# Optimization experiments

Measured on AMD Instinct MI355X. Metric: run time of the kernel, lower is better.

Reference implementation:

```python
import jax, jax.numpy as jnp
import numpy as np

N_HEAD = 16
ROPE_BASE = 10000.0


def _rope_tables(T, head_dim, dtype=jnp.float32):
    inv_freq = 1.0 / (ROPE_BASE ** (jnp.arange(0, head_dim, 2, dtype=jnp.float32) / head_dim))
    t = jnp.arange(T, dtype=jnp.float32)
    freqs = t[:, None] * inv_freq[None, :]          # [T, D/2]
    emb = jnp.concatenate([freqs, freqs], axis=-1)  # [T, D]
    return jnp.cos(emb).astype(dtype), jnp.sin(emb).astype(dtype)


def _rotate_half(x):
    d = x.shape[-1] // 2
    return jnp.concatenate([-x[..., d:], x[..., :d]], axis=-1)


def setup_inputs() -> dict:
    key = jax.random.key(0)
    ks = jax.random.split(key, 5)
    B, T, C = 2, 2048, 2048
    s = 1.0 / np.sqrt(C)
    return {
        "x": jax.random.normal(ks[0], (B, T, C), dtype=jnp.float32),
        "wq": jax.random.normal(ks[1], (C, C), dtype=jnp.float32) * s,
        "wk": jax.random.normal(ks[2], (C, C), dtype=jnp.float32) * s,
        "wv": jax.random.normal(ks[3], (C, C), dtype=jnp.float32) * s,
        "wo": jax.random.normal(ks[4], (C, C), dtype=jnp.float32) * s,
    }


def reference(x, wq, wk, wv, wo):
    B, T, C = x.shape
    H = N_HEAD
    D = C // H

    def heads(y):  # [B,T,C] -> [B,H,T,D]
        return y.reshape(B, T, H, D).transpose(0, 2, 1, 3)

    q = heads(x @ wq)
    k = heads(x @ wk)
    v = heads(x @ wv)

    cos, sin = _rope_tables(T, D, x.dtype)          # [T, D]
    cos = cos[None, None, :, :]
    sin = sin[None, None, :, :]
    q = q * cos + _rotate_half(q) * sin
    k = k * cos + _rotate_half(k) * sin

    scale = 1.0 / np.sqrt(D)
    scores = jnp.einsum('bhqd,bhkd->bhqk', q, k) * scale   # [B,H,T,T]
    causal = jnp.tril(jnp.ones((T, T), dtype=bool))
    scores = jnp.where(causal[None, None, :, :], scores, jnp.finfo(scores.dtype).min)
    attn = jax.nn.softmax(scores, axis=-1)
    y = jnp.einsum('bhqk,bhkd->bhqd', attn, v)             # [B,H,T,D]
    y = y.transpose(0, 2, 1, 3).reshape(B, T, C)
    return y @ wo
```

## Files before the change

### kernel.cpp

```cpp
#include <hip/hip_runtime.h>
#include <hip/hip_bf16.h>
#include <math.h>


#define TT 2048
#define CCn 2048
#define HH 16
#define DD 128
#define MMr 4096
#define NQKV 6144

typedef __attribute__((ext_vector_type(8))) short s16x8;
typedef __attribute__((ext_vector_type(4))) short s16x4;
typedef __attribute__((ext_vector_type(4))) float f32x4;

__device__ __forceinline__ short bf16_of(float f) {
  unsigned u = __float_as_uint(f);
  unsigned r = u + 0x7fffu + ((u >> 16) & 1u);
  return (short)(r >> 16);
}
__device__ __forceinline__ float f_of_bf16(short s) {
  return __uint_as_float(((unsigned)(unsigned short)s) << 16);
}
__device__ __forceinline__ float ex2(float x) { return exp2f(x); }

__device__ __forceinline__ void lds_load16(const void* g, void* l) {
  __builtin_amdgcn_global_load_lds((__attribute__((address_space(1))) void*)g,
                                   (__attribute__((address_space(3))) void*)l,
                                   16, 0, 0);
}

__global__ __launch_bounds__(256) void k_tables(float* __restrict__ cosT,
                                                float* __restrict__ sinT) {
  int idx = blockIdx.x * 256 + threadIdx.x;
  int t = idx >> 6, i = idx & 63;
  float inv = powf(10000.0f, -(float)i * (1.0f / 64.0f));
  float f = (float)t * inv;
  cosT[idx] = cosf(f);
  sinT[idx] = sinf(f);
}

__global__ __launch_bounds__(256) void k_cast_x(const float* __restrict__ x,
                                                short* __restrict__ xb) {
  int i = blockIdx.x * 256 + threadIdx.x;
  f32x4 v = ((const f32x4*)x)[i];
  s16x4 o;
#pragma unroll
  for (int j = 0; j < 4; ++j) o[j] = bf16_of(v[j]);
  ((s16x4*)xb)[i] = o;
}

__global__ __launch_bounds__(256) void k_wtrans4(const float* __restrict__ w0,
                                                 const float* __restrict__ w1,
                                                 const float* __restrict__ w2,
                                                 const float* __restrict__ w3,
                                                 short* __restrict__ wqkvT,
                                                 short* __restrict__ woT) {
  __shared__ float tile[32][33];
  int z = blockIdx.z;
  const float* w = (z == 0) ? w0 : (z == 1) ? w1 : (z == 2) ? w2 : w3;
  short* wt = (z == 3) ? woT : wqkvT + (size_t)z * 2048 * 2048;
  int n0 = blockIdx.x * 32, k0 = blockIdx.y * 32;
  int tx = threadIdx.x & 31, ty = threadIdx.x >> 5;
#pragma unroll
  for (int j = 0; j < 4; ++j) {
    int k = ty * 4 + j;
    tile[k][tx] = w[(size_t)(k0 + k) * CCn + n0 + tx];
  }
  __syncthreads();
#pragma unroll
  for (int j = 0; j < 4; ++j) {
    int n = ty * 4 + j;
    wt[(size_t)(n0 + n) * CCn + k0 + tx] = bf16_of(tile[tx][n]);
  }
}

__global__ __launch_bounds__(256) void k_vtrans(const short* __restrict__ src,
                                                short* __restrict__ dst) {
  __shared__ short tile[32][33];
  int bh = blockIdx.y, b = bh >> 4, h = bh & 15;
  int dt = blockIdx.x & 3, tt = blockIdx.x >> 2;
  int tx = threadIdx.x & 31, ty = threadIdx.x >> 5;
  const short* sp = src + ((size_t)(b * TT + tt * 32)) * NQKV + 4096 + h * DD + dt * 32;
#pragma unroll
  for (int j = 0; j < 4; ++j) {
    int tr = ty * 4 + j;
    tile[tr][tx] = sp[(size_t)tr * NQKV + tx];
  }
  __syncthreads();
  short* dp = dst + ((size_t)(bh * DD + dt * 32)) * TT + tt * 32;
#pragma unroll
  for (int j = 0; j < 4; ++j) {
    int dr = ty * 4 + j;
    dp[(size_t)dr * TT + tx] = tile[tx][dr];
  }
}

__global__ __launch_bounds__(256) void k_rope2(const short* __restrict__ qkv,
                                               const float* __restrict__ cosT,
                                               const float* __restrict__ sinT,
                                               short* __restrict__ Qb,
                                               short* __restrict__ Kb, float kmul) {
  int which = blockIdx.y;
  int coff = which << 11;
  short* dstb = which ? Kb : Qb;
  float mul = which ? kmul : 1.0f;
  int idx = blockIdx.x * 256 + threadIdx.x;
  int i4 = (idx & 15) * 4;
  int h = (idx >> 4) & 15;
  int t = (idx >> 8) & 2047;
  int b = idx >> 19;
  const short* row = qkv + ((size_t)(b * TT + t)) * NQKV + coff + h * DD;
  s16x4 v0 = *(const s16x4*)(row + i4);
  s16x4 v1 = *(const s16x4*)(row + i4 + 64);
  f32x4 c4 = *(const f32x4*)(cosT + t * 64 + i4);
  f32x4 s4 = *(const f32x4*)(sinT + t * 64 + i4);
  s16x4 o0, o1;
#pragma unroll
  for (int j = 0; j < 4; ++j) {
    float a = f_of_bf16(v0[j]), bb = f_of_bf16(v1[j]);
    o0[j] = bf16_of((a * c4[j] - bb * s4[j]) * mul);
    o1[j] = bf16_of((bb * c4[j] + a * s4[j]) * mul);
  }
  short* orow = dstb + ((size_t)((b * HH + h) * TT + t)) * DD;
  *(s16x4*)(orow + i4) = o0;
  *(s16x4*)(orow + i4 + 64) = o1;
}

template <int BF, int BSTG, bool BF16OUT>
__global__ __launch_bounds__(512) void k_gemmW(const short* __restrict__ A,
                                               const short* __restrict__ Bt,
                                               void* __restrict__ Cout,
                                               int M, int N, int K) {
  constexpr int BN = BF * 64;
  constexpr int AH = 4096;
  constexpr int BH = BN * 32;
  __shared__ short smem[4 * AH + 4 * BH];
  const int tid = threadIdx.x, wid = tid >> 6, lane = tid & 63;
  const int wm = wid >> 2, wn = wid & 3;
  const int lr = lane & 15, lk = lane >> 4;
  const int swz = (lk ^ ((lr >> 1) & 3)) * 8;

  int nwg = gridDim.x, orig = blockIdx.x;
  int xcd = orig & 7, bidx = orig >> 3;
  int q = nwg >> 3, rmd = nwg & 7;
  int wg = (xcd < rmd) ? (xcd * (q + 1) + bidx)
                       : (rmd * (q + 1) + (xcd - rmd) * q + bidx);
  const int NBM = M >> 7;
  const int m0 = (wg % NBM) * 128, n0 = (wg / NBM) * BN;

  const int ldswave = (tid & ~63) * 8;

  auto stageA = [&](int buf, int h, int kt) {
    int rr = tid >> 2, cs = tid & 3;
    int cc = cs ^ ((rr >> 1) & 3);
    lds_load16(A + (size_t)(m0 + rr) * K + kt * 64 + h * 32 + cc * 8,
               smem + buf * 2 * AH + h * AH + ldswave);
  };
  auto stageB = [&](int buf, int h, int kt) {
#pragma unroll
    for (int l = 0; l < BSTG; ++l) {
      int lin = l * 512 + tid;
      int rr = lin >> 2, cs = lin & 3;
      int cc = cs ^ ((rr >> 1) & 3);
      lds_load16(Bt + (size_t)(n0 + rr) * K + kt * 64 + h * 32 + cc * 8,
                 smem + 4 * AH + buf * 2 * BH + h * BH + l * 4096 + ldswave);
    }
  };

  s16x8 af[4], bfr[BF / 2];
  f32x4 acc[4][BF] = {};

#define LOAD_A(ks, buf)                                                        \
  _Pragma("unroll") for (int i = 0; i < 4; ++i) af[i] =                        \
      *(const s16x8*)(smem + (buf) * 2 * AH + (ks) * AH +                      \
                      (wm * 64 + i * 16 + lr) * 32 + swz);
#define LOAD_B(ks, bh, buf)                                                    \
  _Pragma("unroll") for (int j = 0; j < BF / 2; ++j) bfr[j] =                  \
      *(const s16x8*)(smem + 4 * AH + (buf) * 2 * BH + (ks) * BH +             \
                      (wn * (BF * 16) + ((bh) * (BF / 2) + j) * 16 + lr) * 32 +\
                      swz);
#define PHASE_MFMA(bh)                                                         \
  __builtin_amdgcn_s_setprio(1);                                               \
  _Pragma("unroll") for (int i = 0; i < 4; ++i)                                \
      _Pragma("unroll") for (int j = 0; j < BF / 2; ++j)                       \
      acc[i][(bh) * (BF / 2) + j] = __builtin_amdgcn_mfma_f32_16x16x32_bf16(   \
          af[i], bfr[j], acc[i][(bh) * (BF / 2) + j], 0, 0, 0);                \
  __builtin_amdgcn_s_setprio(0);
#define VMCNT_N()                                                              \
  if constexpr (BSTG == 3) asm volatile("s_waitcnt vmcnt(4)" ::: "memory");    \
  else asm volatile("s_waitcnt vmcnt(3)" ::: "memory");

  const int nk = K >> 6;
  stageA(0, 0, 0);
  stageB(0, 0, 0);
  stageA(0, 1, 0);
  stageB(0, 1, 0);
  stageA(1, 0, 1);
  stageB(1, 0, 1);
  VMCNT_N();
  __builtin_amdgcn_s_barrier();

#pragma unroll 1
  for (int kt = 0; kt < nk; ++kt) {
    const int buf = kt & 1, nbuf = buf ^ 1;
    const bool s1 = (kt + 1 < nk), s2 = (kt + 2 < nk);
    LOAD_A(0, buf);
    LOAD_B(0, 0, buf);
    if (s1) stageA(nbuf, 1, kt + 1);
    __builtin_amdgcn_s_barrier();
    PHASE_MFMA(0);
    __builtin_amdgcn_s_barrier();
    LOAD_B(0, 1, buf);
    if (s1) stageB(nbuf, 1, kt + 1);
    __builtin_amdgcn_s_barrier();
    PHASE_MFMA(1);
    __builtin_amdgcn_s_barrier();
    LOAD_A(1, buf);
    LOAD_B(1, 0, buf);
    if (s2) stageA(buf, 0, kt + 2);
    __builtin_amdgcn_s_barrier();
    PHASE_MFMA(0);
    __builtin_amdgcn_s_barrier();
    LOAD_B(1, 1, buf);
    if (s2) stageB(buf, 0, kt + 2);
    __builtin_amdgcn_s_barrier();
    PHASE_MFMA(1);
    if (kt < nk - 2) {
      VMCNT_N();
    } else {
      asm volatile("s_waitcnt vmcnt(0)" ::: "memory");
    }
    __builtin_amdgcn_s_barrier();
  }
#undef LOAD_A
#undef LOAD_B
#undef PHASE_MFMA
#undef VMCNT_N

#pragma unroll
  for (int i = 0; i < 4; ++i)
#pragma unroll
    for (int j = 0; j < BF; ++j) {
      int row0 = m0 + wm * 64 + i * 16 + lk * 4;
      int col = n0 + wn * (BF * 16) + j * 16 + lr;
#pragma unroll
      for (int rr = 0; rr < 4; ++rr) {
        if (BF16OUT)
          ((short*)Cout)[(size_t)(row0 + rr) * N + col] = bf16_of(acc[i][j][rr]);
        else
          ((float*)Cout)[(size_t)(row0 + rr) * N + col] = acc[i][j][rr];
      }
    }
}

__global__ __launch_bounds__(256) void k_attn(const short* __restrict__ Qb,
                                              const short* __restrict__ Kb,
                                              const short* __restrict__ Vt,
                                              short* __restrict__ yb) {
  __shared__ short Ks[2][64 * 128];
  __shared__ short Vs[128 * 64];
  __shared__ short Ps[4][16 * 72];
  const int tid = threadIdx.x, wid = tid >> 6, lane = tid & 63;
  const int lr = lane & 15, lk = lane >> 4;
  const int bh = blockIdx.y, bx = blockIdx.x;
  const size_t baseQK = (size_t)bh * TT * DD;
  const int b = bh >> 4, h = bh & 15;

  auto stageK = [&](int bi, int kt2) {
#pragma unroll
    for (int it = 0; it < 4; ++it) {
      int ch = it * 256 + tid;
      int r = ch >> 4, cc = ch & 15;
      int cs = cc ^ (r & 7);
      lds_load16(Kb + baseQK + (size_t)(kt2 * 64 + r) * DD + cs * 8,
                 &Ks[bi][(size_t)(it * 256 + wid * 64) * 8]);
    }
  };
  auto stageV = [&](int kt2) {
#pragma unroll
    for (int it = 0; it < 4; ++it) {
      int ch = it * 256 + tid;
      int d = ch >> 3, kc = ch & 7;
      int cs = kc ^ (d & 7);
      lds_load16(Vt + baseQK + (size_t)d * TT + kt2 * 64 + cs * 8,
                 &Vs[(size_t)(it * 256 + wid * 64) * 8]);
    }
  };

#pragma unroll 1
  for (int pass = 0; pass < 2; ++pass) {
    const int qt = pass ? (31 - bx) : bx;
    const int q0 = qt * 64;
    const int qg = q0 + wid * 16 + lr;
    s16x8 qf[4];
#pragma unroll
    for (int ds = 0; ds < 4; ++ds)
      qf[ds] = *(const s16x8*)(Qb + baseQK + (size_t)qg * DD + (ds * 4 + lk) * 8);

    float mrun = -3.0e38f, lrun = 0.f;
    f32x4 yacc[8] = {};

    const int nkt = qt + 1;
    stageK(0, 0);
    stageV(0);
    __syncthreads();
    int buf = 0;
#pragma unroll 1
    for (int kt = 0; kt < nkt; ++kt) {
      if (kt + 1 < nkt) stageK(buf ^ 1, kt + 1);
      f32x4 sf[4] = {};
#pragma unroll
      for (int sub = 0; sub < 4; ++sub) {
        int kr = sub * 16 + lr;
#pragma unroll
        for (int ds = 0; ds < 4; ++ds) {
          int cc = (ds * 4 + lk) ^ (kr & 7);
          s16x8 kf = *(const s16x8*)(&Ks[buf][kr * 128 + cc * 8]);
          sf[sub] = __builtin_amdgcn_mfma_f32_16x16x32_bf16(kf, qf[ds], sf[sub], 0, 0, 0);
        }
      }
      const int kvbase = kt * 64;
      if (kvbase + 63 > q0 + wid * 16) {
#pragma unroll
        for (int sub = 0; sub < 4; ++sub)
#pragma unroll
          for (int r = 0; r < 4; ++r) {
            int kv = kvbase + sub * 16 + lk * 4 + r;
            if (kv > qg) sf[sub][r] = -3.0e38f;
          }
      }
      float tmax = -3.0e38f;
#pragma unroll
      for (int sub = 0; sub < 4; ++sub)
#pragma unroll
        for (int r = 0; r < 4; ++r) tmax = fmaxf(tmax, sf[sub][r]);
      tmax = fmaxf(tmax, __shfl_xor(tmax, 16, 64));
      tmax = fmaxf(tmax, __shfl_xor(tmax, 32, 64));
      if (!__all(tmax <= mrun + 11.0f)) {
        float mnew = fmaxf(mrun, tmax);
        float alpha = ex2(mrun - mnew);
        mrun = mnew;
        lrun *= alpha;
        float ar[4];
#pragma unroll
        for (int r = 0; r < 4; ++r) ar[r] = __shfl(alpha, lk * 4 + r, 64);
#pragma unroll
        for (int dn = 0; dn < 8; ++dn)
#pragma unroll
          for (int r = 0; r < 4; ++r) yacc[dn][r] *= ar[r];
      }
      float psum = 0.f;
#pragma unroll
      for (int sub = 0; sub < 4; ++sub) {
        s16x4 pq;
#pragma unroll
        for (int r = 0; r < 4; ++r) {
          float p = ex2(sf[sub][r] - mrun);
          psum += p;
          pq[r] = bf16_of(p);
        }
        *(s16x4*)(&Ps[wid][lr * 72 + sub * 16 + lk * 4]) = pq;
      }
      psum += __shfl_xor(psum, 16, 64);
      psum += __shfl_xor(psum, 32, 64);
      lrun += psum;
      __syncthreads();
      s16x8 pf0 = *(const s16x8*)(&Ps[wid][lr * 72 + lk * 8]);
      s16x8 pf1 = *(const s16x8*)(&Ps[wid][lr * 72 + 32 + lk * 8]);
#pragma unroll
      for (int dn = 0; dn < 8; ++dn) {
        int d = dn * 16 + lr;
        s16x8 vf0 = *(const s16x8*)(&Vs[d * 64 + (lk ^ (d & 7)) * 8]);
        yacc[dn] = __builtin_amdgcn_mfma_f32_16x16x32_bf16(pf0, vf0, yacc[dn], 0, 0, 0);
        s16x8 vf1 = *(const s16x8*)(&Vs[d * 64 + ((4 + lk) ^ (d & 7)) * 8]);
        yacc[dn] = __builtin_amdgcn_mfma_f32_16x16x32_bf16(pf1, vf1, yacc[dn], 0, 0, 0);
      }
      __syncthreads();
      if (kt + 1 < nkt) stageV(kt + 1);
      buf ^= 1;
    }
    float linv = 1.f / lrun;
    float lr4[4];
#pragma unroll
    for (int r = 0; r < 4; ++r) lr4[r] = __shfl(linv, lk * 4 + r, 64);
#pragma unroll
    for (int dn = 0; dn < 8; ++dn)
#pragma unroll
      for (int r = 0; r < 4; ++r) {
        int t = q0 + wid * 16 + lk * 4 + r;
        int c = h * DD + dn * 16 + lr;
        yb[((size_t)(b * TT + t)) * CCn + c] = bf16_of(yacc[dn][r] * lr4[r]);
      }
  }
}

extern "C" void kernel_launch(void* const* d_in, const int* in_sizes, int n_in,
                              void* d_out, int out_size, void* d_ws, size_t ws_size,
                              hipStream_t stream) {
  const float* x = (const float*)d_in[0];
  const float* wq = (const float*)d_in[1];
  const float* wk = (const float*)d_in[2];
  const float* wv = (const float*)d_in[3];
  const float* wo = (const float*)d_in[4];
  float* out = (float*)d_out;
  char* ws = (char*)d_ws;

  short* xb = (short*)(ws + 0);
  short* wqkvT = (short*)(ws + 16777216);
  short* woT = (short*)(ws + 41943040);
  short* qkv = (short*)(ws + 50331648);
  short* yb = (short*)(ws + 50331648);
  short* Qb = (short*)(ws + 100663296);
  short* Kb = (short*)(ws + 117440512);
  short* Vt = (short*)(ws + 134217728);
  float* cosT = (float*)(ws + 150994944);
  float* sinT = (float*)(ws + 151519232);

  const float kmul = 1.4426950408889634f / sqrtf(128.0f);

  k_tables<<<512, 256, 0, stream>>>(cosT, sinT);
  k_cast_x<<<8192, 256, 0, stream>>>(x, xb);
  k_wtrans4<<<dim3(64, 64, 4), 256, 0, stream>>>(wq, wk, wv, wo, wqkvT, woT);

  k_gemmW<6, 3, true><<<512, 512, 0, stream>>>(xb, wqkvT, qkv, MMr, NQKV, CCn);

  k_rope2<<<dim3(4096, 2), 256, 0, stream>>>(qkv, cosT, sinT, Qb, Kb, kmul);
  k_vtrans<<<dim3(256, 32), 256, 0, stream>>>(qkv, Vt);

  k_attn<<<dim3(16, 32), 256, 0, stream>>>(Qb, Kb, Vt, yb);

  k_gemmW<4, 2, false><<<256, 512, 0, stream>>>(yb, woT, out, MMr, CCn, CCn);
}
```

Baseline: 401.4 us.

## Replace GEMM kernel with 256-row tiles and restructured double-buffered pipeline

Swaps the 128-row GEMM kernel for one with 256-row M tiles, where each wave computes 128x(WNF*16) outputs. It stages A and B halves in a new interleaved prefetch schedule with explicit lgkmcnt waits before each MFMA phase. For the QKV projection the tile goes from 128x384 to 256x256, giving 384 workgroups. For the output projection it goes from 128x256 to 256x128. The aim is more operand reuse per LDS load and less barrier overhead per MFMA, at the cost of more accumulator registers, more LDS and fewer or differently balanced workgroups.

```diff
diff --git a/kernel.cpp b/kernel.cpp
--- a/kernel.cpp
+++ b/kernel.cpp
@@ -127,15 +127,16 @@
   *(s16x4*)(orow + i4 + 64) = o1;
 }
 
-template <int BF, int BSTG, bool BF16OUT>
-__global__ __launch_bounds__(512) void k_gemmW(const short* __restrict__ A,
-                                               const short* __restrict__ Bt,
-                                               void* __restrict__ Cout,
-                                               int M, int N, int K) {
-  constexpr int BN = BF * 64;
-  constexpr int AH = 4096;
-  constexpr int BH = BN * 32;
-  __shared__ short smem[4 * AH + 4 * BH];
+template <int WNF, bool BF16OUT>
+__global__ __launch_bounds__(512) void k_g8(const short* __restrict__ A,
+                                            const short* __restrict__ Bt,
+                                            void* __restrict__ Cout,
+                                            int M, int N, int K) {
+  constexpr int BN = WNF * 64;
+  constexpr int BHS = BN * 32;
+  constexpr int NBL = WNF / 2;
+  constexpr int VMN = 2 + WNF;
+  __shared__ short smem[32768 + 4 * BHS];
   const int tid = threadIdx.x, wid = tid >> 6, lane = tid & 63;
   const int wm = wid >> 2, wn = wid & 3;
   const int lr = lane & 15, lk = lane >> 4;
@@ -146,110 +147,116 @@
   int q = nwg >> 3, rmd = nwg & 7;
   int wg = (xcd < rmd) ? (xcd * (q + 1) + bidx)
                        : (rmd * (q + 1) + (xcd - rmd) * q + bidx);
-  const int NBM = M >> 7;
-  const int m0 = (wg % NBM) * 128, n0 = (wg / NBM) * BN;
-
-  const int ldswave = (tid & ~63) * 8;
-
-  auto stageA = [&](int buf, int h, int kt) {
-    int rr = tid >> 2, cs = tid & 3;
-    int cc = cs ^ ((rr >> 1) & 3);
-    lds_load16(A + (size_t)(m0 + rr) * K + kt * 64 + h * 32 + cc * 8,
-               smem + buf * 2 * AH + h * AH + ldswave);
+  const int NBM = M >> 8;
+  const int m0 = (wg % NBM) * 256, n0 = (wg / NBM) * BN;
+
+  auto stageA = [&](int buf, int ks, int kt) {
+#pragma unroll
+    for (int l = 0; l < 2; ++l) {
+      int lin = l * 512 + tid;
+      int row = lin >> 2;
+      int cc = (lin & 3) ^ ((row >> 1) & 3);
+      lds_load16(A + (size_t)(m0 + row) * K + kt * 64 + ks * 32 + cc * 8,
+                 smem + buf * 16384 + ks * 8192 + lin * 8);
+    }
   };
-  auto stageB = [&](int buf, int h, int kt) {
-#pragma unroll
-    for (int l = 0; l < BSTG; ++l) {
+  auto stageB = [&](int buf, int ks, int kt) {
+#pragma unroll
+    for (int l = 0; l < NBL; ++l) {
       int lin = l * 512 + tid;
-      int rr = lin >> 2, cs = lin & 3;
-      int cc = cs ^ ((rr >> 1) & 3);
-      lds_load16(Bt + (size_t)(n0 + rr) * K + kt * 64 + h * 32 + cc * 8,
-                 smem + 4 * AH + buf * 2 * BH + h * BH + l * 4096 + ldswave);
+      int row = lin >> 2;
+      int cc = (lin & 3) ^ ((row >> 1) & 3);
+      lds_load16(Bt + (size_t)(n0 + row) * K + kt * 64 + ks * 32 + cc * 8,
+                 smem + 32768 + buf * 2 * BHS + ks * BHS + lin * 8);
     }
   };
 
-  s16x8 af[4], bfr[BF / 2];
-  f32x4 acc[4][BF] = {};
-
-#define LOAD_A(ks, buf)                                                        \
+  s16x8 af[4], bfr[WNF];
+  f32x4 acc[8][WNF] = {};
+
+#define LDA(BUF, KS, MH)                                                       \
   _Pragma("unroll") for (int i = 0; i < 4; ++i) af[i] =                        \
-      *(const s16x8*)(smem + (buf) * 2 * AH + (ks) * AH +                      \
-                      (wm * 64 + i * 16 + lr) * 32 + swz);
-#define LOAD_B(ks, bh, buf)                                                    \
-  _Pragma("unroll") for (int j = 0; j < BF / 2; ++j) bfr[j] =                  \
-      *(const s16x8*)(smem + 4 * AH + (buf) * 2 * BH + (ks) * BH +             \
-                      (wn * (BF * 16) + ((bh) * (BF / 2) + j) * 16 + lr) * 32 +\
-                      swz);
-#define PHASE_MFMA(bh)                                                         \
+      *(const s16x8*)(smem + (BUF) * 16384 + (KS) * 8192 +                     \
+                      (wm * 128 + (MH) * 64 + i * 16 + lr) * 32 + swz);
+#define LDB(BUF, KS)                                                           \
+  _Pragma("unroll") for (int j = 0; j < WNF; ++j) bfr[j] =                     \
+      *(const s16x8*)(smem + 32768 + (BUF) * 2 * BHS + (KS) * BHS +            \
+                      (wn * (WNF * 16) + j * 16 + lr) * 32 + swz);
+#define BAR_MFMA(MH)                                                           \
+  __builtin_amdgcn_s_barrier();                                                \
+  asm volatile("s_waitcnt lgkmcnt(0)" ::: "memory");                           \
   __builtin_amdgcn_s_setprio(1);                                               \
   _Pragma("unroll") for (int i = 0; i < 4; ++i)                                \
-      _Pragma("unroll") for (int j = 0; j < BF / 2; ++j)                       \
-      acc[i][(bh) * (BF / 2) + j] = __builtin_amdgcn_mfma_f32_16x16x32_bf16(   \
-          af[i], bfr[j], acc[i][(bh) * (BF / 2) + j], 0, 0, 0);                \
+      _Pragma("unroll") for (int j = 0; j < WNF; ++j)                          \
+      acc[(MH) * 4 + i][j] = __builtin_amdgcn_mfma_f32_16x16x32_bf16(          \
+          af[i], bfr[j], acc[(MH) * 4 + i][j], 0, 0, 0);                       \
   __builtin_amdgcn_s_setprio(0);
-#define VMCNT_N()                                                              \
-  if constexpr (BSTG == 3) asm volatile("s_waitcnt vmcnt(4)" ::: "memory");    \
-  else asm volatile("s_waitcnt vmcnt(3)" ::: "memory");
-
-  const int nk = K >> 6;
-  stageA(0, 0, 0);
-  stageB(0, 0, 0);
-  stageA(0, 1, 0);
-  stageB(0, 1, 0);
-  stageA(1, 0, 1);
-  stageB(1, 0, 1);
-  VMCNT_N();
+#define VMW(cond)                                                              \
+  if (cond) { asm volatile("s_waitcnt vmcnt(%0)" ::"i"(VMN) : "memory"); }     \
+  else      { asm volatile("s_waitcnt vmcnt(0)" ::: "memory"); }
+
+  const int nk = K >> 6, niter = nk >> 1;
+  stageB(0, 0, 0); stageA(0, 0, 0); stageB(0, 1, 0); stageA(0, 1, 0);
+  stageB(1, 0, 1); stageA(1, 0, 1); stageB(1, 1, 1);
+  asm volatile("s_waitcnt vmcnt(%0)" ::"i"(VMN) : "memory");
   __builtin_amdgcn_s_barrier();
 
 #pragma unroll 1
-  for (int kt = 0; kt < nk; ++kt) {
-    const int buf = kt & 1, nbuf = buf ^ 1;
-    const bool s1 = (kt + 1 < nk), s2 = (kt + 2 < nk);
-    LOAD_A(0, buf);
-    LOAD_B(0, 0, buf);
-    if (s1) stageA(nbuf, 1, kt + 1);
-    __builtin_amdgcn_s_barrier();
-    PHASE_MFMA(0);
-    __builtin_amdgcn_s_barrier();
-    LOAD_B(0, 1, buf);
-    if (s1) stageB(nbuf, 1, kt + 1);
-    __builtin_amdgcn_s_barrier();
-    PHASE_MFMA(1);
-    __builtin_amdgcn_s_barrier();
-    LOAD_A(1, buf);
-    LOAD_B(1, 0, buf);
-    if (s2) stageA(buf, 0, kt + 2);
-    __builtin_amdgcn_s_barrier();
-    PHASE_MFMA(0);
-    __builtin_amdgcn_s_barrier();
-    LOAD_B(1, 1, buf);
-    if (s2) stageB(buf, 0, kt + 2);
-    __builtin_amdgcn_s_barrier();
-    PHASE_MFMA(1);
-    if (kt < nk - 2) {
-      VMCNT_N();
-    } else {
-      asm volatile("s_waitcnt vmcnt(0)" ::: "memory");
-    }
-    __builtin_amdgcn_s_barrier();
-  }
-#undef LOAD_A
-#undef LOAD_B
-#undef PHASE_MFMA
-#undef VMCNT_N
-
-#pragma unroll
-  for (int i = 0; i < 4; ++i)
-#pragma unroll
-    for (int j = 0; j < BF; ++j) {
-      int row0 = m0 + wm * 64 + i * 16 + lk * 4;
-      int col = n0 + wn * (BF * 16) + j * 16 + lr;
+  for (int it = 0; it < niter; ++it) {
+    const int kt1 = 2 * it + 1, kt2 = 2 * it + 2, kt3 = 2 * it + 3;
+    const bool s2 = kt2 < nk, s3 = kt3 < nk;
+    LDA(0, 0, 0); LDB(0, 0);
+    stageA(1, 1, kt1);
+    BAR_MFMA(0);
+    __builtin_amdgcn_s_barrier();
+    LDA(0, 0, 1);
+    if (s2) stageB(0, 0, kt2);
+    BAR_MFMA(1);
+    __builtin_amdgcn_s_barrier();
+    LDA(0, 1, 0); LDB(0, 1);
+    if (s2) stageA(0, 0, kt2);
+    BAR_MFMA(0);
+    __builtin_amdgcn_s_barrier();
+    LDA(0, 1, 1);
+    if (s2) stageB(0, 1, kt2);
+    BAR_MFMA(1);
+    VMW(s2);
+    __builtin_amdgcn_s_barrier();
+    LDA(1, 0, 0); LDB(1, 0);
+    if (s2) stageA(0, 1, kt2);
+    BAR_MFMA(0);
+    __builtin_amdgcn_s_barrier();
+    LDA(1, 0, 1);
+    if (s3) stageB(1, 0, kt3);
+    BAR_MFMA(1);
+    __builtin_amdgcn_s_barrier();
+    LDA(1, 1, 0); LDB(1, 1);
+    if (s3) stageA(1, 0, kt3);
+    BAR_MFMA(0);
+    __builtin_amdgcn_s_barrier();
+    LDA(1, 1, 1);
+    if (s3) stageB(1, 1, kt3);
+    BAR_MFMA(1);
+    VMW(s3);
+    __builtin_amdgcn_s_barrier();
+  }
+#undef LDA
+#undef LDB
+#undef BAR_MFMA
+#undef VMW
+
+#pragma unroll
+  for (int f = 0; f < 8; ++f)
+#pragma unroll
+    for (int j = 0; j < WNF; ++j) {
+      int row0 = m0 + wm * 128 + (f >> 2) * 64 + (f & 3) * 16 + lk * 4;
+      int col = n0 + wn * (WNF * 16) + j * 16 + lr;
 #pragma unroll
       for (int rr = 0; rr < 4; ++rr) {
         if (BF16OUT)
-          ((short*)Cout)[(size_t)(row0 + rr) * N + col] = bf16_of(acc[i][j][rr]);
+          ((short*)Cout)[(size_t)(row0 + rr) * N + col] = bf16_of(acc[f][j][rr]);
         else
-          ((float*)Cout)[(size_t)(row0 + rr) * N + col] = acc[i][j][rr];
+          ((float*)Cout)[(size_t)(row0 + rr) * N + col] = acc[f][j][rr];
       }
     }
 }
@@ -423,12 +430,12 @@
   k_cast_x<<<8192, 256, 0, stream>>>(x, xb);
   k_wtrans4<<<dim3(64, 64, 4), 256, 0, stream>>>(wq, wk, wv, wo, wqkvT, woT);
 
-  k_gemmW<6, 3, true><<<512, 512, 0, stream>>>(xb, wqkvT, qkv, MMr, NQKV, CCn);
+  k_g8<4, true><<<384, 512, 0, stream>>>(xb, wqkvT, qkv, MMr, NQKV, CCn);
 
   k_rope2<<<dim3(4096, 2), 256, 0, stream>>>(qkv, cosT, sinT, Qb, Kb, kmul);
   k_vtrans<<<dim3(256, 32), 256, 0, stream>>>(qkv, Vt);
 
   k_attn<<<dim3(16, 32), 256, 0, stream>>>(Qb, Kb, Vt, yb);
 
-  k_gemmW<4, 2, false><<<256, 512, 0, stream>>>(yb, woT, out, MMr, CCn, CCn);
-}
+  k_g8<2, false><<<256, 512, 0, stream>>>(yb, woT, out, MMr, CCn, CCn);
+}
```

After: 405.1 us. Within noise of the previous version (+0.9%).
